# Optimization experiments

Hardware: AMD Instinct MI355X
Metric: run time of the kernel (lower is better)

## Reference

```python
import jax, jax.numpy as jnp
import numpy as np

B, S, D_IN, D_H, D_FF, E, D_OUT = 1024, 2048, 4, 16, 32, 8, 4

def setup_inputs() -> dict:
    key = jax.random.key(0)
    ks = jax.random.split(key, 8)
    return {
        "x":       jax.random.normal(ks[0], (B, S, D_IN), dtype=jnp.float32),
        "embed_w": jax.random.normal(ks[1], (D_H, D_IN), dtype=jnp.float32) / np.sqrt(D_IN),
        "embed_b": jnp.zeros((D_H,), dtype=jnp.float32),
        "gate_w":  jax.random.normal(ks[2], (D_H, E), dtype=jnp.float32) / np.sqrt(D_H),
        "wi":      jax.random.normal(ks[3], (E, D_H, D_FF), dtype=jnp.float32) / np.sqrt(D_H),
        "wo":      jax.random.normal(ks[4], (E, D_FF, D_H), dtype=jnp.float32) / np.sqrt(D_FF),
        "proj_w":  jax.random.normal(ks[5], (D_OUT, D_H), dtype=jnp.float32) / np.sqrt(D_H),
        "proj_b":  jnp.zeros((D_OUT,), dtype=jnp.float32),
    }

def reference(x, embed_w, embed_b, gate_w, wi, wo, proj_w, proj_b):
    # test_embed: Linear(4, 16)
    h = x @ embed_w.T + embed_b                      # [B, S, 16]
    t = h.reshape(-1, D_H)                           # [T, 16], T = B*S

    # SparseMLP top-1 router (softmax gate, no bias)
    probs = jax.nn.softmax(t @ gate_w, axis=-1)      # [T, E]
    top_idx = jnp.argmax(probs, axis=-1)             # [T] expert id
    top_p = jnp.max(probs, axis=-1)                  # [T] combine weight

    # Expert FFN (gelu MLP, no bias); small fixed loop over E=8 experts,
    # masked combine honors the top-1 dispatch structure.
    out = jnp.zeros_like(t)
    for e in range(E):
        y_e = jax.nn.gelu(t @ wi[e]) @ wo[e]         # [T, 16]
        out = out + jnp.where((top_idx == e)[:, None], y_e, 0.0)
    out = out * top_p[:, None]                       # combine with gate prob
    out = out.reshape(B, S, D_H)

    # proj: Linear(16, 4)
    return out @ proj_w.T + proj_b                   # [B, S, 4]
```

## Files before the change

### kernel.cpp

```cpp
#include <hip/hip_runtime.h>

constexpr int TOK     = 1024 * 2048;
constexpr int TPB     = 256;
constexpr int TOK_PB  = 1024;
constexpr int ITERS   = TOK_PB / TPB;
constexpr int NBLK    = TOK / TOK_PB;

typedef float f32x4 __attribute__((ext_vector_type(4)));

constexpr int WS_FLOATS = 2348;

__global__ void setup_fused(
    const float* __restrict__ ew,
    const float* __restrict__ eb,
    const float* __restrict__ gw,
    const float* __restrict__ wi,
    const float* __restrict__ wo,
    const float* __restrict__ pw,
    const float* __restrict__ pb,
    float* __restrict__ ws)
{
    int idx = blockIdx.x * blockDim.x + threadIdx.x;
    if (idx >= WS_FLOATS) return;
    float v = 0.0f;
    if (idx < 32) {
        int k = idx >> 3, j = idx & 7;
        for (int i = 0; i < 16; ++i) v += ew[i * 4 + k] * gw[i * 8 + j];
    } else if (idx < 40) {
        int j = idx - 32;
        for (int i = 0; i < 16; ++i) v += eb[i] * gw[i * 8 + j];
    } else if (idx < 1064) {
        int r = idx - 40; int e = r >> 7, k = (r >> 5) & 3, f = r & 31;
        for (int i = 0; i < 16; ++i) v += ew[i * 4 + k] * wi[(e * 16 + i) * 32 + f];
    } else if (idx < 1320) {
        int r = idx - 1064; int e = r >> 5, f = r & 31;
        for (int i = 0; i < 16; ++i) v += eb[i] * wi[(e * 16 + i) * 32 + f];
    } else if (idx < 2344) {
        int r = idx - 1320; int e = r >> 7, f = (r >> 2) & 31, o = r & 3;
        for (int i = 0; i < 16; ++i) v += wo[(e * 32 + f) * 16 + i] * pw[o * 16 + i];
    } else {
        v = pb[idx - 2344];
    }
    ws[idx] = v;
}

__device__ __forceinline__ f32x4 splat4(float s) { return (f32x4){s, s, s, s}; }

__global__ __launch_bounds__(256) void moe_main(
    const float* __restrict__ x,
    const float* __restrict__ ws,
    float* __restrict__ out)
{
    __shared__ __align__(16) f32x4 s_x[TOK_PB];
    __shared__ float           s_p[TOK_PB];
    __shared__ unsigned short  s_sid[TOK_PB];
    __shared__ int             s_cnt[8];
    __shared__ int             s_base[8];
    __shared__ __align__(16) float sWf[8 * 128];
    __shared__ __align__(16) float sUb[8 * 32];
    __shared__ __align__(16) float sPf[8 * 128];

    const int tid  = threadIdx.x;
    const int lane = tid & 63;
    const unsigned long long lt_mask = (lane == 63) ? 0x7fffffffffffffffull
                                                    : ((1ull << lane) - 1ull);

    if (tid < 8) s_cnt[tid] = 0;
    {
        int i = tid;
        #pragma unroll
        for (int rep = 0; rep < 4; ++rep, i += 256) {
            sWf[i] = ws[40 + i];
            sPf[i] = ws[1320 + i];
        }
        sUb[tid] = ws[1064 + tid];
    }

    const int gbase = blockIdx.x * TOK_PB;
    const f32x4* __restrict__ x4 = (const f32x4*)x;
    f32x4* __restrict__ o4       = (f32x4*)out;

    f32x4 Gr[8];
    #pragma unroll
    for (int q = 0; q < 8; ++q) Gr[q] = ((const f32x4*)ws)[q];
    const f32x4 w_gb0 = ((const f32x4*)ws)[8];
    const f32x4 w_gb1 = ((const f32x4*)ws)[9];
    const f32x4 w_pb  = ((const f32x4*)(ws + 2344))[0];

    constexpr float LOG2E  = 1.4426950408889634f;
    constexpr float GELU_K = 2.3025850929940457f;
    constexpr float GELU_B = 0.044715f;
    const f32x4 one4 = splat4(1.0f);

    __syncthreads();

    int e_arr[ITERS], pos_arr[ITERS];

    #pragma unroll
    for (int it = 0; it < ITERS; ++it) {
        const int t_loc = it * TPB + tid;
        f32x4 xv = x4[gbase + t_loc];
        s_x[t_loc] = xv;

        f32x4 ga = w_gb0, gb2 = w_gb1;
        #pragma unroll
        for (int k = 0; k < 4; ++k) {
            f32x4 xs = splat4(xv[k]);
            ga  = __builtin_elementwise_fma(xs, Gr[2 * k],     ga);
            gb2 = __builtin_elementwise_fma(xs, Gr[2 * k + 1], gb2);
        }
        float g[8] = {ga[0], ga[1], ga[2], ga[3], gb2[0], gb2[1], gb2[2], gb2[3]};

        float gmax = g[0]; int e = 0;
        #pragma unroll
        for (int j = 1; j < 8; ++j)
            if (g[j] > gmax) { gmax = g[j]; e = j; }
        float ssum = 0.0f;
        #pragma unroll
        for (int j = 0; j < 8; ++j)
            ssum += __builtin_amdgcn_exp2f((g[j] - gmax) * LOG2E);
        s_p[t_loc] = __builtin_amdgcn_rcpf(ssum);

        int pos_w = 0, my_cnt = 0;
        #pragma unroll
        for (int j = 0; j < 8; ++j) {
            unsigned long long bj = __ballot(e == j);
            int pc_lt = __popcll(bj & lt_mask);
            int pc    = __popcll(bj);
            if (e == j)    pos_w  = pc_lt;
            if (lane == j) my_cnt = pc;
        }
        int base_w = 0;
        if (lane < 8) base_w = atomicAdd(&s_cnt[lane], my_cnt);
        int base = __shfl(base_w, e, 64);
        e_arr[it]   = e;
        pos_arr[it] = base + pos_w;
    }
    __syncthreads();

    if (tid == 0) {
        int run = 0;
        #pragma unroll
        for (int j = 0; j < 8; ++j) { s_base[j] = run; run += s_cnt[j]; }
    }
    __syncthreads();

    #pragma unroll
    for (int it = 0; it < ITERS; ++it) {
        const int t_loc = it * TPB + tid;
        const int slot  = s_base[e_arr[it]] + pos_arr[it];
        s_sid[slot] = (unsigned short)(t_loc | (e_arr[it] << 10));
    }
    __syncthreads();

    #pragma unroll 1
    for (int it = 0; it < ITERS; ++it) {
        const unsigned v = s_sid[it * TPB + tid];
        const int sid = (int)(v & 1023u);
        const int e   = (int)(v >> 10);

        f32x4 xv = s_x[sid];
        float tp = s_p[sid];

        const f32x4* __restrict__ wf4 = (const f32x4*)(sWf + e * 128);
        const f32x4* __restrict__ ub4 = (const f32x4*)(sUb + e * 32);
        const f32x4* __restrict__ pf4 = (const f32x4*)(sPf + e * 128);

        f32x4 U[8];
        #pragma unroll
        for (int q = 0; q < 8; ++q) U[q] = ub4[q];
        #pragma unroll
        for (int k = 0; k < 4; ++k) {
            f32x4 xs = splat4(xv[k]);
            #pragma unroll
            for (int q = 0; q < 8; ++q)
                U[q] = __builtin_elementwise_fma(xs, wf4[k * 8 + q], U[q]);
        }

        #pragma unroll
        for (int q = 0; q < 8; ++q) {
            f32x4 vv = U[q];
            f32x4 m  = __builtin_elementwise_fma(vv * splat4(GELU_B), vv, one4);
            f32x4 a  = (vv * splat4(GELU_K)) * m;
            f32x4 tt;
            #pragma unroll
            for (int c = 0; c < 4; ++c) tt[c] = __builtin_amdgcn_exp2f(a[c]);
            tt = tt + one4;
            f32x4 r;
            #pragma unroll
            for (int c = 0; c < 4; ++c) r[c] = __builtin_amdgcn_rcpf(tt[c]);
            U[q] = __builtin_elementwise_fma(-vv, r, vv);
        }

        f32x4 acc = splat4(0.0f);
        #pragma unroll
        for (int q = 0; q < 8; ++q) {
            #pragma unroll
            for (int c = 0; c < 4; ++c)
                acc = __builtin_elementwise_fma(splat4(U[q][c]), pf4[q * 4 + c], acc);
        }
        s_x[sid] = __builtin_elementwise_fma(splat4(tp), acc, w_pb);
    }
    __syncthreads();

    #pragma unroll
    for (int it = 0; it < ITERS; ++it) {
        const int t_loc = it * TPB + tid;
        o4[gbase + t_loc] = s_x[t_loc];
    }
}

extern "C" void kernel_launch(void* const* d_in, const int* in_sizes, int n_in,
                              void* d_out, int out_size, void* d_ws, size_t ws_size,
                              hipStream_t stream) {
    const float* x  = (const float*)d_in[0];
    const float* ew = (const float*)d_in[1];
    const float* eb = (const float*)d_in[2];
    const float* gw = (const float*)d_in[3];
    const float* wi = (const float*)d_in[4];
    const float* wo = (const float*)d_in[5];
    const float* pw = (const float*)d_in[6];
    const float* pb = (const float*)d_in[7];
    float* ws  = (float*)d_ws;
    float* out = (float*)d_out;

    setup_fused<<<(WS_FLOATS + 255) / 256, 256, 0, stream>>>(ew, eb, gw, wi, wo, pw, pb, ws);
    moe_main<<<NBLK, TPB, 0, stream>>>(x, ws, out);
}
```

Measured before the change: 50.11 us.

## Process eight sorted tokens per thread, reusing expert weight chunks across them

After: 105.0 us. 110% more time.

```diff
diff --git a/kernel.cpp b/kernel.cpp
--- a/kernel.cpp
+++ b/kernel.cpp
@@ -2,8 +2,9 @@
 
 constexpr int TOK     = 1024 * 2048;
 constexpr int TPB     = 256;
-constexpr int TOK_PB  = 1024;
-constexpr int ITERS   = TOK_PB / TPB;
+constexpr int TOK_PB  = 2048;
+constexpr int P1_IT   = TOK_PB / TPB;
+constexpr int G       = 8;
 constexpr int NBLK    = TOK / TOK_PB;
 
 typedef float f32x4 __attribute__((ext_vector_type(4)));
@@ -51,11 +52,11 @@
     const float* __restrict__ ws,
     float* __restrict__ out)
 {
-    __shared__ __align__(16) f32x4 s_x[TOK_PB];
-    __shared__ float           s_p[TOK_PB];
-    __shared__ unsigned short  s_sid[TOK_PB];
-    __shared__ int             s_cnt[8];
-    __shared__ int             s_base[8];
+    __shared__ __align__(16) f32x4          s_x[TOK_PB];
+    __shared__ float                        s_p[TOK_PB];
+    __shared__ __align__(16) unsigned short s_sid[TOK_PB];
+    __shared__ int s_cnt[8];
+    __shared__ int s_base[8];
     __shared__ __align__(16) float sWf[8 * 128];
     __shared__ __align__(16) float sUb[8 * 32];
     __shared__ __align__(16) float sPf[8 * 128];
@@ -94,10 +95,10 @@
 
     __syncthreads();
 
-    int e_arr[ITERS], pos_arr[ITERS];
-
-    #pragma unroll
-    for (int it = 0; it < ITERS; ++it) {
+    int e_arr[P1_IT], pos_arr[P1_IT];
+
+    #pragma unroll
+    for (int it = 0; it < P1_IT; ++it) {
         const int t_loc = it * TPB + tid;
         f32x4 xv = x4[gbase + t_loc];
         s_x[t_loc] = xv;
@@ -146,65 +147,91 @@
     __syncthreads();
 
     #pragma unroll
-    for (int it = 0; it < ITERS; ++it) {
+    for (int it = 0; it < P1_IT; ++it) {
         const int t_loc = it * TPB + tid;
         const int slot  = s_base[e_arr[it]] + pos_arr[it];
-        s_sid[slot] = (unsigned short)(t_loc | (e_arr[it] << 10));
-    }
-    __syncthreads();
-
-    #pragma unroll 1
-    for (int it = 0; it < ITERS; ++it) {
-        const unsigned v = s_sid[it * TPB + tid];
-        const int sid = (int)(v & 1023u);
-        const int e   = (int)(v >> 10);
-
-        f32x4 xv = s_x[sid];
-        float tp = s_p[sid];
-
-        const f32x4* __restrict__ wf4 = (const f32x4*)(sWf + e * 128);
-        const f32x4* __restrict__ ub4 = (const f32x4*)(sUb + e * 32);
-        const f32x4* __restrict__ pf4 = (const f32x4*)(sPf + e * 128);
-
-        f32x4 U[8];
-        #pragma unroll
-        for (int q = 0; q < 8; ++q) U[q] = ub4[q];
-        #pragma unroll
-        for (int k = 0; k < 4; ++k) {
-            f32x4 xs = splat4(xv[k]);
+        s_sid[slot] = (unsigned short)(t_loc | (e_arr[it] << 11));
+    }
+    __syncthreads();
+
+    {
+        const int g0 = tid * G;
+        uint4 meta = *(const uint4*)&s_sid[g0];
+        int sid[G], eg[G];
+        {
+            unsigned mw[4] = {meta.x, meta.y, meta.z, meta.w};
             #pragma unroll
-            for (int q = 0; q < 8; ++q)
-                U[q] = __builtin_elementwise_fma(xs, wf4[k * 8 + q], U[q]);
-        }
-
-        #pragma unroll
-        for (int q = 0; q < 8; ++q) {
-            f32x4 vv = U[q];
-            f32x4 m  = __builtin_elementwise_fma(vv * splat4(GELU_B), vv, one4);
-            f32x4 a  = (vv * splat4(GELU_K)) * m;
-            f32x4 tt;
+            for (int h = 0; h < 4; ++h) {
+                sid[2 * h]     = (int)(mw[h] & 2047u);
+                eg[2 * h]      = (int)((mw[h] >> 11) & 7u);
+                sid[2 * h + 1] = (int)((mw[h] >> 16) & 2047u);
+                eg[2 * h + 1]  = (int)((mw[h] >> 27) & 7u);
+            }
+        }
+
+        f32x4 xr[G];
+        #pragma unroll
+        for (int g = 0; g < G; ++g) xr[g] = s_x[sid[g]];
+        f32x4 acc[G];
+        #pragma unroll
+        for (int g = 0; g < G; ++g) acc[g] = splat4(0.0f);
+
+        #pragma unroll 1
+        for (int c = 0; c < 8; ++c) {
+            f32x4 wf0, wf1, wf2, wf3, ubv, pf0, pf1, pf2, pf3;
+            int cur_e = eg[0];
+            auto load_w = [&](int e) {
+                const float* wfp = sWf + e * 128 + c * 4;
+                wf0 = *(const f32x4*)(wfp + 0);
+                wf1 = *(const f32x4*)(wfp + 32);
+                wf2 = *(const f32x4*)(wfp + 64);
+                wf3 = *(const f32x4*)(wfp + 96);
+                ubv = *(const f32x4*)(sUb + e * 32 + c * 4);
+                const float* pfp = sPf + e * 128 + c * 16;
+                pf0 = *(const f32x4*)(pfp + 0);
+                pf1 = *(const f32x4*)(pfp + 4);
+                pf2 = *(const f32x4*)(pfp + 8);
+                pf3 = *(const f32x4*)(pfp + 12);
+            };
+            load_w(cur_e);
+
             #pragma unroll
-            for (int c = 0; c < 4; ++c) tt[c] = __builtin_amdgcn_exp2f(a[c]);
-            tt = tt + one4;
-            f32x4 r;
-            #pragma unroll
-            for (int c = 0; c < 4; ++c) r[c] = __builtin_amdgcn_rcpf(tt[c]);
-            U[q] = __builtin_elementwise_fma(-vv, r, vv);
-        }
-
-        f32x4 acc = splat4(0.0f);
-        #pragma unroll
-        for (int q = 0; q < 8; ++q) {
-            #pragma unroll
-            for (int c = 0; c < 4; ++c)
-                acc = __builtin_elementwise_fma(splat4(U[q][c]), pf4[q * 4 + c], acc);
-        }
-        s_x[sid] = __builtin_elementwise_fma(splat4(tp), acc, w_pb);
-    }
-    __syncthreads();
-
-    #pragma unroll
-    for (int it = 0; it < ITERS; ++it) {
+            for (int g = 0; g < G; ++g) {
+                if (eg[g] != cur_e) { cur_e = eg[g]; load_w(cur_e); }
+                f32x4 U = ubv;
+                U = __builtin_elementwise_fma(splat4(xr[g][0]), wf0, U);
+                U = __builtin_elementwise_fma(splat4(xr[g][1]), wf1, U);
+                U = __builtin_elementwise_fma(splat4(xr[g][2]), wf2, U);
+                U = __builtin_elementwise_fma(splat4(xr[g][3]), wf3, U);
+
+                f32x4 m  = __builtin_elementwise_fma(U * splat4(GELU_B), U, one4);
+                f32x4 a  = (U * splat4(GELU_K)) * m;
+                f32x4 tt;
+                #pragma unroll
+                for (int q = 0; q < 4; ++q) tt[q] = __builtin_amdgcn_exp2f(a[q]);
+                tt = tt + one4;
+                f32x4 r;
+                #pragma unroll
+                for (int q = 0; q < 4; ++q) r[q] = __builtin_amdgcn_rcpf(tt[q]);
+                f32x4 Ug = __builtin_elementwise_fma(-U, r, U);
+
+                acc[g] = __builtin_elementwise_fma(splat4(Ug[0]), pf0, acc[g]);
+                acc[g] = __builtin_elementwise_fma(splat4(Ug[1]), pf1, acc[g]);
+                acc[g] = __builtin_elementwise_fma(splat4(Ug[2]), pf2, acc[g]);
+                acc[g] = __builtin_elementwise_fma(splat4(Ug[3]), pf3, acc[g]);
+            }
+        }
+
+        #pragma unroll
+        for (int g = 0; g < G; ++g) {
+            float tp = s_p[sid[g]];
+            s_x[sid[g]] = __builtin_elementwise_fma(splat4(tp), acc[g], w_pb);
+        }
+    }
+    __syncthreads();
+
+    #pragma unroll
+    for (int it = 0; it < P1_IT; ++it) {
         const int t_loc = it * TPB + tid;
         o4[gbase + t_loc] = s_x[t_loc];
     }
```

## Pad expert groups to wavefront size and read expert weights via scalar loads

Applied to the files above, without the earlier changes.

New measurement: 62.03 us. 1.24x slower.

```diff
diff --git a/kernel.cpp b/kernel.cpp
--- a/kernel.cpp
+++ b/kernel.cpp
@@ -2,9 +2,10 @@
 
 constexpr int TOK     = 1024 * 2048;
 constexpr int TPB     = 256;
-constexpr int TOK_PB  = 1024;
-constexpr int ITERS   = TOK_PB / TPB;
+constexpr int TOK_PB  = 2048;
+constexpr int P1_IT   = TOK_PB / TPB;
 constexpr int NBLK    = TOK / TOK_PB;
+constexpr int SID_CAP = 2560;
 
 typedef float f32x4 __attribute__((ext_vector_type(4)));
 
@@ -51,14 +52,12 @@
     const float* __restrict__ ws,
     float* __restrict__ out)
 {
-    __shared__ __align__(16) f32x4 s_x[TOK_PB];
-    __shared__ float           s_p[TOK_PB];
-    __shared__ unsigned short  s_sid[TOK_PB];
-    __shared__ int             s_cnt[8];
-    __shared__ int             s_base[8];
-    __shared__ __align__(16) float sWf[8 * 128];
-    __shared__ __align__(16) float sUb[8 * 32];
-    __shared__ __align__(16) float sPf[8 * 128];
+    __shared__ __align__(16) f32x4          s_x[TOK_PB];
+    __shared__ float                        s_p[TOK_PB];
+    __shared__ __align__(16) unsigned short s_sid[SID_CAP];
+    __shared__ int s_cnt[8];
+    __shared__ int s_base[8];
+    __shared__ int s_padtot;
 
     const int tid  = threadIdx.x;
     const int lane = tid & 63;
@@ -66,15 +65,6 @@
                                                     : ((1ull << lane) - 1ull);
 
     if (tid < 8) s_cnt[tid] = 0;
-    {
-        int i = tid;
-        #pragma unroll
-        for (int rep = 0; rep < 4; ++rep, i += 256) {
-            sWf[i] = ws[40 + i];
-            sPf[i] = ws[1320 + i];
-        }
-        sUb[tid] = ws[1064 + tid];
-    }
 
     const int gbase = blockIdx.x * TOK_PB;
     const f32x4* __restrict__ x4 = (const f32x4*)x;
@@ -94,10 +84,10 @@
 
     __syncthreads();
 
-    int e_arr[ITERS], pos_arr[ITERS];
-
-    #pragma unroll
-    for (int it = 0; it < ITERS; ++it) {
+    int e_arr[P1_IT], pos_arr[P1_IT];
+
+    #pragma unroll
+    for (int it = 0; it < P1_IT; ++it) {
         const int t_loc = it * TPB + tid;
         f32x4 xv = x4[gbase + t_loc];
         s_x[t_loc] = xv;
@@ -141,70 +131,105 @@
     if (tid == 0) {
         int run = 0;
         #pragma unroll
-        for (int j = 0; j < 8; ++j) { s_base[j] = run; run += s_cnt[j]; }
-    }
-    __syncthreads();
-
-    #pragma unroll
-    for (int it = 0; it < ITERS; ++it) {
+        for (int j = 0; j < 8; ++j) {
+            s_base[j] = run;
+            run += (s_cnt[j] + 63) & ~63;
+        }
+        s_padtot = run;
+    }
+    __syncthreads();
+
+    const int padtot = s_padtot;
+
+    #pragma unroll 1
+    for (int s = tid; s < padtot; s += TPB) {
+        int e = 0;
+        #pragma unroll
+        for (int j = 1; j < 8; ++j)
+            if (s >= s_base[j]) e = j;
+        s_sid[s] = (unsigned short)((e << 11) | (1u << 14));
+    }
+    __syncthreads();
+
+    #pragma unroll
+    for (int it = 0; it < P1_IT; ++it) {
         const int t_loc = it * TPB + tid;
         const int slot  = s_base[e_arr[it]] + pos_arr[it];
-        s_sid[slot] = (unsigned short)(t_loc | (e_arr[it] << 10));
+        s_sid[slot] = (unsigned short)(t_loc | (e_arr[it] << 11));
     }
     __syncthreads();
 
     #pragma unroll 1
-    for (int it = 0; it < ITERS; ++it) {
-        const unsigned v = s_sid[it * TPB + tid];
-        const int sid = (int)(v & 1023u);
-        const int e   = (int)(v >> 10);
+    for (int s = tid; s < padtot; s += TPB) {
+        const unsigned v = s_sid[s];
+        const int sid   = (int)(v & 2047u);
+        const bool live = (v & (1u << 14)) == 0;
+        const int eu = __builtin_amdgcn_readfirstlane((int)((v >> 11) & 7u));
 
         f32x4 xv = s_x[sid];
-        float tp = s_p[sid];
-
-        const f32x4* __restrict__ wf4 = (const f32x4*)(sWf + e * 128);
-        const f32x4* __restrict__ ub4 = (const f32x4*)(sUb + e * 32);
-        const f32x4* __restrict__ pf4 = (const f32x4*)(sPf + e * 128);
-
-        f32x4 U[8];
-        #pragma unroll
-        for (int q = 0; q < 8; ++q) U[q] = ub4[q];
-        #pragma unroll
-        for (int k = 0; k < 4; ++k) {
-            f32x4 xs = splat4(xv[k]);
+
+        const float* __restrict__ wf = ws + 40   + eu * 128;
+        const float* __restrict__ ub = ws + 1064 + eu * 32;
+        const float* __restrict__ pf = ws + 1320 + eu * 128;
+
+        f32x4 acc = splat4(0.0f);
+
+        #pragma unroll 1
+        for (int c = 0; c < 4; ++c) {
+            f32x4 Ua = *(const f32x4*)(ub + c * 8);
+            f32x4 Ub = *(const f32x4*)(ub + c * 8 + 4);
             #pragma unroll
-            for (int q = 0; q < 8; ++q)
-                U[q] = __builtin_elementwise_fma(xs, wf4[k * 8 + q], U[q]);
-        }
-
-        #pragma unroll
-        for (int q = 0; q < 8; ++q) {
-            f32x4 vv = U[q];
-            f32x4 m  = __builtin_elementwise_fma(vv * splat4(GELU_B), vv, one4);
-            f32x4 a  = (vv * splat4(GELU_K)) * m;
-            f32x4 tt;
+            for (int k = 0; k < 4; ++k) {
+                const float* w = wf + k * 32 + c * 8;
+                f32x4 xs = splat4(xv[k]);
+                Ua = __builtin_elementwise_fma(xs, *(const f32x4*)(w),     Ua);
+                Ub = __builtin_elementwise_fma(xs, *(const f32x4*)(w + 4), Ub);
+            }
+
+            {
+                f32x4 m  = __builtin_elementwise_fma(Ua * splat4(GELU_B), Ua, one4);
+                f32x4 a  = (Ua * splat4(GELU_K)) * m;
+                f32x4 tt;
+                #pragma unroll
+                for (int q = 0; q < 4; ++q) tt[q] = __builtin_amdgcn_exp2f(a[q]);
+                tt = tt + one4;
+                f32x4 r;
+                #pragma unroll
+                for (int q = 0; q < 4; ++q) r[q] = __builtin_amdgcn_rcpf(tt[q]);
+                Ua = __builtin_elementwise_fma(-Ua, r, Ua);
+            }
+            {
+                f32x4 m  = __builtin_elementwise_fma(Ub * splat4(GELU_B), Ub, one4);
+                f32x4 a  = (Ub * splat4(GELU_K)) * m;
+                f32x4 tt;
+                #pragma unroll
+                for (int q = 0; q < 4; ++q) tt[q] = __builtin_amdgcn_exp2f(a[q]);
+                tt = tt + one4;
+                f32x4 r;
+                #pragma unroll
+                for (int q = 0; q < 4; ++q) r[q] = __builtin_amdgcn_rcpf(tt[q]);
+                Ub = __builtin_elementwise_fma(-Ub, r, Ub);
+            }
+
+            const float* pfc = pf + c * 32;
             #pragma unroll
-            for (int c = 0; c < 4; ++c) tt[c] = __builtin_amdgcn_exp2f(a[c]);
-            tt = tt + one4;
-            f32x4 r;
-            #pragma unroll
-            for (int c = 0; c < 4; ++c) r[c] = __builtin_amdgcn_rcpf(tt[c]);
-            U[q] = __builtin_elementwise_fma(-vv, r, vv);
-        }
-
-        f32x4 acc = splat4(0.0f);
-        #pragma unroll
-        for (int q = 0; q < 8; ++q) {
-            #pragma unroll
-            for (int c = 0; c < 4; ++c)
-                acc = __builtin_elementwise_fma(splat4(U[q][c]), pf4[q * 4 + c], acc);
-        }
-        s_x[sid] = __builtin_elementwise_fma(splat4(tp), acc, w_pb);
-    }
-    __syncthreads();
-
-    #pragma unroll
-    for (int it = 0; it < ITERS; ++it) {
+            for (int f = 0; f < 4; ++f) {
+                acc = __builtin_elementwise_fma(splat4(Ua[f]),
+                        *(const f32x4*)(pfc + f * 4), acc);
+                acc = __builtin_elementwise_fma(splat4(Ub[f]),
+                        *(const f32x4*)(pfc + 16 + f * 4), acc);
+            }
+        }
+
+        if (live) {
+            float tp = s_p[sid];
+            s_x[sid] = __builtin_elementwise_fma(splat4(tp), acc, w_pb);
+        }
+    }
+    __syncthreads();
+
+    #pragma unroll
+    for (int it = 0; it < P1_IT; ++it) {
         const int t_loc = it * TPB + tid;
         o4[gbase + t_loc] = s_x[t_loc];
     }
```
